# Kernel optimization log

Measured on AMD Instinct MI355X. Metric: run time of the kernel, lower is better.

Reference implementation:

```python
import jax, jax.numpy as jnp
import numpy as np

BIG = 1e10  # diagonal mask to exclude self-distance
EPS = 1e-8

def setup_inputs() -> dict:
    key = jax.random.key(0)
    N = 16384
    point_cloud = jax.random.normal(key, (N, 2), dtype=jnp.float32) * 10.0
    return {"point_cloud": point_cloud}

def reference(point_cloud):
    # point_cloud: (N, 2)
    N = point_cloud.shape[0]
    # Pairwise squared distances via the Gram trick (avoids (N,N,2) intermediate).
    sq = jnp.sum(point_cloud * point_cloud, axis=1)              # (N,)
    d2 = sq[:, None] + sq[None, :] - 2.0 * (point_cloud @ point_cloud.T)  # (N,N)
    d2 = jnp.maximum(d2, 0.0)
    d2 = d2 + jnp.eye(N, dtype=d2.dtype) * BIG                   # mask diagonal
    # ESDF: distance to nearest other point (sqrt of min squared distance,
    # equivalent to min of distances since sqrt is monotone).
    esdf = jnp.sqrt(jnp.min(d2, axis=1))                          # (N,)
    nearest = jnp.argmin(d2, axis=1)                              # (N,) int
    # Gradient direction: unit vector from nearest neighbor toward the point.
    direction = point_cloud - point_cloud[nearest]                # (N,2)
    nrm = jnp.linalg.norm(direction, axis=1, keepdims=True)       # (N,1)
    grads = direction / (nrm + EPS)                               # (N,2)
    gx, gy = grads[:, 0], grads[:, 1]
    mu = jnp.stack([gx, -gx, gy, -gy], axis=0)                    # (4,N)
    lam = jnp.stack([gx, gy, esdf / 10.0], axis=0)                # (3,N)
    return mu, lam
```

## Files before the change

kernel.cpp:

```cpp
#include <hip/hip_runtime.h>
#include <math.h>

#define TPB 256
#define JWIN 512
#define BIGV 1e10f
#define EPSV 1e-8f

__global__ void esdf_prep(const float2* __restrict__ pc,
                          float* __restrict__ sq,
                          unsigned long long* __restrict__ key, int n) {
#pragma clang fp contract(off)
    int i = blockIdx.x * blockDim.x + threadIdx.x;
    if (i < n) {
        float2 p = pc[i];
        float xx = p.x * p.x;
        float yy = p.y * p.y;
        sq[i] = xx + yy;
        key[i] = ~0ull;
    }
}

__global__ __launch_bounds__(TPB)
void esdf_nn(const float2* __restrict__ pc,
             const float* __restrict__ sq,
             unsigned long long* __restrict__ key, int n) {
#pragma clang fp contract(off)
    const int tid    = threadIdx.x;
    const int jparts = n / JWIN;
    const int qblk   = blockIdx.x / jparts;
    const int jpart  = blockIdx.x % jparts;
    const int qbase  = qblk * TPB;
    const int jbase  = jpart * JWIN;
    const bool selfwin = ((qbase & ~(JWIN - 1)) == jbase);
    const int qw = qbase + (tid & 192);

    __shared__ float sXl[JWIN];
    __shared__ float sYl[JWIN];
    __shared__ float sSql[JWIN];
#pragma unroll
    for (int h = 0; h < JWIN / TPB; ++h) {
        int t = h * TPB + tid;
        float2 p = pc[jbase + t];
        sXl[t] = p.x;
        sYl[t] = p.y;
        sSql[t] = sq[jbase + t];
    }

    const int q = qbase + tid;
    float2 pq = pc[q];
    const float xq = pq.x, yq = pq.y, sqq = sq[q];
    __syncthreads();

    float best  = BIGV;
    int   btile = 0;

    for (int jt = 0; jt < JWIN; jt += 8) {
        const int j0 = jbase + jt;
        float4 xA = *(const float4*)&sXl[jt];
        float4 xB = *(const float4*)&sXl[jt + 4];
        float4 yA = *(const float4*)&sYl[jt];
        float4 yB = *(const float4*)&sYl[jt + 4];
        float4 sA = *(const float4*)&sSql[jt];
        float4 sB = *(const float4*)&sSql[jt + 4];
        float xs[8] = {xA.x, xA.y, xA.z, xA.w, xB.x, xB.y, xB.z, xB.w};
        float ys[8] = {yA.x, yA.y, yA.z, yA.w, yB.x, yB.y, yB.z, yB.w};
        float ss[8] = {sA.x, sA.y, sA.z, sA.w, sB.x, sB.y, sB.z, sB.w};

        float d[8];
#pragma unroll
        for (int k = 0; k < 8; ++k) {
            float dot = fmaf(ys[k], yq, xs[k] * xq);
            float s   = sqq + ss[k];
            float v   = fmaf(-2.0f, dot, s);
            d[k] = fmaxf(v, 0.0f);
        }

        if (selfwin && ((j0 & ~63) == qw)) {
#pragma unroll
            for (int k = 0; k < 8; ++k)
                if (j0 + k == q) d[k] = BIGV;
        }

        float m01 = fminf(fminf(d[0], d[1]), d[2]);
        float m23 = fminf(fminf(d[3], d[4]), d[5]);
        float m45 = fminf(d[6], d[7]);
        float tmin = fminf(fminf(m01, m23), m45);

        const int tileId = j0 >> 3;
        bool lt = tmin < best;
        best  = fminf(best, tmin);
        btile = lt ? tileId : btile;
    }

    unsigned long long kk =
        ((unsigned long long)__float_as_uint(best) << 32) | (unsigned)btile;
    unsigned long long cur = *(const volatile unsigned long long*)&key[q];
    if (kk < cur) atomicMin(&key[q], kk);
}

__global__ void esdf_finalize(const float2* __restrict__ pc,
                              const float* __restrict__ sq,
                              const unsigned long long* __restrict__ key,
                              float* __restrict__ out, int n) {
#pragma clang fp contract(off)
    int q = blockIdx.x * blockDim.x + threadIdx.x;
    if (q >= n) return;
    unsigned long long k = key[q];
    float best = __uint_as_float((unsigned)(k >> 32));
    int   j0   = ((int)(k & 0xffffffffull)) << 3;

    float2 pq = pc[q];
    const float xq = pq.x, yq = pq.y, sqq = sq[q];

    int ix = j0;
    bool found = false;
#pragma unroll
    for (int kk = 0; kk < 8; ++kk) {
        int j = j0 + kk;
        float2 pj = pc[j];
        float dot = fmaf(pj.y, yq, pj.x * xq);
        float s   = sqq + sq[j];
        float v   = fmaf(-2.0f, dot, s);
        v = fmaxf(v, 0.0f);
        if (!found && j != q && v == best) { ix = j; found = true; }
    }

    float esdf = sqrtf(best);
    float2 pn = pc[ix];
    float dx = xq - pn.x;
    float dy = yq - pn.y;
    float a  = dx * dx;
    float c2 = dy * dy;
    float nrm = sqrtf(a + c2);
    float inv = nrm + EPSV;
    float gx = dx / inv;
    float gy = dy / inv;
    out[0 * n + q] = gx;
    out[1 * n + q] = -gx;
    out[2 * n + q] = gy;
    out[3 * n + q] = -gy;
    out[4 * n + q] = gx;
    out[5 * n + q] = gy;
    out[6 * n + q] = esdf / 10.0f;
}

extern "C" void kernel_launch(void* const* d_in, const int* in_sizes, int n_in,
                              void* d_out, int out_size, void* d_ws, size_t ws_size,
                              hipStream_t stream) {
    const float2* pc = (const float2*)d_in[0];
    float* out = (float*)d_out;
    const int n = in_sizes[0] / 2;

    float* sq = (float*)d_ws;
    unsigned long long* key = (unsigned long long*)(sq + n);

    const int jparts = n / JWIN;
    const int qblks  = n / TPB;

    esdf_prep<<<(n + 255) / 256, 256, 0, stream>>>(pc, sq, key, n);
    esdf_nn<<<qblks * jparts, TPB, 0, stream>>>(pc, sq, key, n);
    esdf_finalize<<<(n + 255) / 256, 256, 0, stream>>>(pc, sq, key, out, n);
}
```

Baseline: 48.36 us.

## Register-block two queries per thread and drop the squared-norm prep kernel

```diff
diff --git a/kernel.cpp b/kernel.cpp
--- a/kernel.cpp
+++ b/kernel.cpp
@@ -2,57 +2,53 @@
 #include <math.h>
 
 #define TPB 256
-#define JWIN 512
+#define QPT 2
+#define QSPAN (TPB * QPT)
+#define JWIN 256
 #define BIGV 1e10f
 #define EPSV 1e-8f
 
-__global__ void esdf_prep(const float2* __restrict__ pc,
-                          float* __restrict__ sq,
-                          unsigned long long* __restrict__ key, int n) {
-#pragma clang fp contract(off)
-    int i = blockIdx.x * blockDim.x + threadIdx.x;
-    if (i < n) {
-        float2 p = pc[i];
-        float xx = p.x * p.x;
-        float yy = p.y * p.y;
-        sq[i] = xx + yy;
-        key[i] = ~0ull;
-    }
-}
-
 __global__ __launch_bounds__(TPB)
 void esdf_nn(const float2* __restrict__ pc,
-             const float* __restrict__ sq,
              unsigned long long* __restrict__ key, int n) {
 #pragma clang fp contract(off)
     const int tid    = threadIdx.x;
     const int jparts = n / JWIN;
     const int qblk   = blockIdx.x / jparts;
     const int jpart  = blockIdx.x % jparts;
-    const int qbase  = qblk * TPB;
+    const int qbase  = qblk * QSPAN;
     const int jbase  = jpart * JWIN;
-    const bool selfwin = ((qbase & ~(JWIN - 1)) == jbase);
-    const int qw = qbase + (tid & 192);
+    const bool self0 = (jbase == qbase);
+    const bool self1 = (jbase == qbase + TPB);
 
     __shared__ float sXl[JWIN];
     __shared__ float sYl[JWIN];
     __shared__ float sSql[JWIN];
-#pragma unroll
-    for (int h = 0; h < JWIN / TPB; ++h) {
-        int t = h * TPB + tid;
-        float2 p = pc[jbase + t];
-        sXl[t] = p.x;
-        sYl[t] = p.y;
-        sSql[t] = sq[jbase + t];
+    if (tid < JWIN / 2) {
+        float4 p4 = ((const float4*)pc)[(jbase >> 1) + tid];
+        int t2 = tid * 2;
+        sXl[t2]     = p4.x;
+        sYl[t2]     = p4.y;
+        float xx0 = p4.x * p4.x, yy0 = p4.y * p4.y;
+        sSql[t2]    = xx0 + yy0;
+        sXl[t2 + 1] = p4.z;
+        sYl[t2 + 1] = p4.w;
+        float xx1 = p4.z * p4.z, yy1 = p4.w * p4.w;
+        sSql[t2 + 1] = xx1 + yy1;
     }
 
-    const int q = qbase + tid;
-    float2 pq = pc[q];
-    const float xq = pq.x, yq = pq.y, sqq = sq[q];
+    const int iq0 = qbase + tid;
+    const int iq1 = qbase + TPB + tid;
+    float2 p0 = pc[iq0], p1 = pc[iq1];
+    const float x0 = p0.x, y0 = p0.y;
+    const float s0 = (x0 * x0) + (y0 * y0);
+    const float x1 = p1.x, y1 = p1.y;
+    const float s1 = (x1 * x1) + (y1 * y1);
     __syncthreads();
 
-    float best  = BIGV;
-    int   btile = 0;
+    float best0 = BIGV, best1 = BIGV;
+    int   bt0 = 0, bt1 = 0;
+    const int w0 = iq0 >> 6, w1 = iq1 >> 6;
 
     for (int jt = 0; jt < JWIN; jt += 8) {
         const int j0 = jbase + jt;
@@ -65,41 +61,65 @@
         float xs[8] = {xA.x, xA.y, xA.z, xA.w, xB.x, xB.y, xB.z, xB.w};
         float ys[8] = {yA.x, yA.y, yA.z, yA.w, yB.x, yB.y, yB.z, yB.w};
         float ss[8] = {sA.x, sA.y, sA.z, sA.w, sB.x, sB.y, sB.z, sB.w};
+        const int tileId = j0 >> 3;
 
-        float d[8];
+        {
+            float d[8];
 #pragma unroll
-        for (int k = 0; k < 8; ++k) {
-            float dot = fmaf(ys[k], yq, xs[k] * xq);
-            float s   = sqq + ss[k];
-            float v   = fmaf(-2.0f, dot, s);
-            d[k] = fmaxf(v, 0.0f);
+            for (int k = 0; k < 8; ++k) {
+                float dot = fmaf(ys[k], y0, xs[k] * x0);
+                float s   = s0 + ss[k];
+                float v   = fmaf(-2.0f, dot, s);
+                d[k] = fmaxf(v, 0.0f);
+            }
+            if (self0 && ((j0 >> 6) == w0)) {
+#pragma unroll
+                for (int k = 0; k < 8; ++k)
+                    if (j0 + k == iq0) d[k] = BIGV;
+            }
+            float m01 = fminf(fminf(d[0], d[1]), d[2]);
+            float m23 = fminf(fminf(d[3], d[4]), d[5]);
+            float m45 = fminf(d[6], d[7]);
+            float tmin = fminf(fminf(m01, m23), m45);
+            bool lt = tmin < best0;
+            best0 = fminf(best0, tmin);
+            bt0   = lt ? tileId : bt0;
         }
-
-        if (selfwin && ((j0 & ~63) == qw)) {
+        {
+            float d[8];
 #pragma unroll
-            for (int k = 0; k < 8; ++k)
-                if (j0 + k == q) d[k] = BIGV;
+            for (int k = 0; k < 8; ++k) {
+                float dot = fmaf(ys[k], y1, xs[k] * x1);
+                float s   = s1 + ss[k];
+                float v   = fmaf(-2.0f, dot, s);
+                d[k] = fmaxf(v, 0.0f);
+            }
+            if (self1 && ((j0 >> 6) == w1)) {
+#pragma unroll
+                for (int k = 0; k < 8; ++k)
+                    if (j0 + k == iq1) d[k] = BIGV;
+            }
+            float m01 = fminf(fminf(d[0], d[1]), d[2]);
+            float m23 = fminf(fminf(d[3], d[4]), d[5]);
+            float m45 = fminf(d[6], d[7]);
+            float tmin = fminf(fminf(m01, m23), m45);
+            bool lt = tmin < best1;
+            best1 = fminf(best1, tmin);
+            bt1   = lt ? tileId : bt1;
         }
-
-        float m01 = fminf(fminf(d[0], d[1]), d[2]);
-        float m23 = fminf(fminf(d[3], d[4]), d[5]);
-        float m45 = fminf(d[6], d[7]);
-        float tmin = fminf(fminf(m01, m23), m45);
-
-        const int tileId = j0 >> 3;
-        bool lt = tmin < best;
-        best  = fminf(best, tmin);
-        btile = lt ? tileId : btile;
     }
 
-    unsigned long long kk =
-        ((unsigned long long)__float_as_uint(best) << 32) | (unsigned)btile;
-    unsigned long long cur = *(const volatile unsigned long long*)&key[q];
-    if (kk < cur) atomicMin(&key[q], kk);
+    unsigned long long k0 =
+        ((unsigned long long)__float_as_uint(best0) << 32) | (unsigned)bt0;
+    unsigned long long k1 =
+        ((unsigned long long)__float_as_uint(best1) << 32) | (unsigned)bt1;
+    unsigned long long c0 = *(const volatile unsigned long long*)&key[iq0];
+    if (k0 < c0) atomicMin(&key[iq0], k0);
+    unsigned long long c1 = *(const volatile unsigned long long*)&key[iq1];
+    if (k1 < c1) atomicMin(&key[iq1], k1);
 }
 
 __global__ void esdf_finalize(const float2* __restrict__ pc,
-                              const float* __restrict__ sq,
                               const unsigned long long* __restrict__ key,
                               float* __restrict__ out, int n) {
 #pragma clang fp contract(off)
@@ -110,7 +130,8 @@
     int   j0   = ((int)(k & 0xffffffffull)) << 3;
 
     float2 pq = pc[q];
-    const float xq = pq.x, yq = pq.y, sqq = sq[q];
+    const float xq = pq.x, yq = pq.y;
+    const float sqq = (xq * xq) + (yq * yq);
 
     int ix = j0;
     bool found = false;
@@ -118,8 +139,9 @@
     for (int kk = 0; kk < 8; ++kk) {
         int j = j0 + kk;
         float2 pj = pc[j];
+        float sj  = (pj.x * pj.x) + (pj.y * pj.y);
         float dot = fmaf(pj.y, yq, pj.x * xq);
-        float s   = sqq + sq[j];
+        float s   = sqq + sj;
         float v   = fmaf(-2.0f, dot, s);
         v = fmaxf(v, 0.0f);
         if (!found && j != q && v == best) { ix = j; found = true; }
@@ -151,13 +173,12 @@
     float* out = (float*)d_out;
     const int n = in_sizes[0] / 2;
 
-    float* sq = (float*)d_ws;
-    unsigned long long* key = (unsigned long long*)(sq + n);
+    unsigned long long* key = (unsigned long long*)d_ws;
+    hipMemsetAsync(key, 0xFF, n * sizeof(unsigned long long), stream);
 
     const int jparts = n / JWIN;
-    const int qblks  = n / TPB;
+    const int qblks  = n / QSPAN;
 
-    esdf_prep<<<(n + 255) / 256, 256, 0, stream>>>(pc, sq, key, n);
-    esdf_nn<<<qblks * jparts, TPB, 0, stream>>>(pc, sq, key, n);
-    esdf_finalize<<<(n + 255) / 256, 256, 0, stream>>>(pc, sq, key, out, n);
+    esdf_nn<<<qblks * jparts, TPB, 0, stream>>>(pc, key, n);
+    esdf_finalize<<<(n + 255) / 256, 256, 0, stream>>>(pc, key, out, n);
 }
```

New measurement: 48.36 us (median of 2 runs). No clear change (-0.0%).
